# Optimization experiments

Measured on AMD Instinct MI355X. Metric: run time of the kernel, lower is better.

The kernel has to match this reference:

```python
import jax, jax.numpy as jnp
import numpy as np

CAT_SIZES = [31360, 6807, 18, 94]
TOTAL = int(sum(CAT_SIZES))          # 38279
EMB = 128
N_FIELDS = len(CAT_SIZES)
D_IN = N_FIELDS * EMB                # 512 (num_features is empty)
MLP_DIMS = [2048, 1024, 512]
B = 16384
OFFSETS = np.concatenate([[0], np.cumsum(CAT_SIZES)[:-1]]).astype(np.int32)


def setup_inputs() -> dict:
    key = jax.random.key(0)
    ks = jax.random.split(key, 20)
    # x holds raw per-field category ids stored as float32 (as the torch model expects)
    cols = [jax.random.randint(ks[i], (B,), 0, s) for i, s in enumerate(CAT_SIZES)]
    x = jnp.stack(cols, axis=1).astype(jnp.float32)

    bias = jnp.zeros((1,), jnp.float32)
    fc = jax.random.uniform(ks[4], (TOTAL, 1), dtype=jnp.float32)          # nn.Parameter(torch.rand)
    emb_table = jax.random.normal(ks[5], (TOTAL, EMB), dtype=jnp.float32)  # nn.Embedding default N(0,1)

    dims = [D_IN] + MLP_DIMS + [1]
    params = {}
    for i in range(len(dims) - 1):
        fan_in = dims[i]
        bound = 1.0 / np.sqrt(fan_in)
        params[f"W{i+1}"] = jax.random.uniform(ks[6 + 2 * i], (dims[i], dims[i + 1]), jnp.float32, -bound, bound)
        params[f"b{i+1}"] = jax.random.uniform(ks[7 + 2 * i], (dims[i + 1],), jnp.float32, -bound, bound)

    return dict(x=x, bias=bias, fc=fc, emb_table=emb_table, **params)


def reference(x, bias, fc, emb_table, W1, b1, W2, b2, W3, b3, W4, b4):
    cat = x.astype(jnp.int32)                       # [B, F] raw per-field ids
    b = cat.shape[0]

    # embedding lookup with RAW (un-offset) ids, faithful to the original code
    embed_x = emb_table[cat].reshape(b, -1)          # [B, F*EMB]

    # one_hot(offset ids) @ fc  ==  sum_f fc[offset ids]  (offset ranges disjoint)
    gidx = cat + jnp.asarray(OFFSETS)                # [B, F] global ids
    lin = jnp.sum(fc[gidx, 0], axis=1)               # [B]
    fm_y = bias + lin                                # [B]

    # FM term: embed_x is 2-D, so sum over dim=1 collapses features;
    # the keepdim sum over dim=-1 then collapses the BATCH dim to shape (1,)
    # (a quirk of the original code that we reproduce exactly)
    square_of_sum = jnp.sum(embed_x, axis=1) ** 2    # [B]
    sum_of_square = jnp.sum(embed_x ** 2, axis=1)    # [B]
    fm_y = fm_y + 0.5 * jnp.sum(square_of_sum - sum_of_square, axis=-1, keepdims=True)  # [B]
    fm_y = fm_y[:, None]                             # [B,1]

    # MLP (eval mode: dropout is identity)
    h = embed_x
    for W, bb in ((W1, b1), (W2, b2), (W3, b3)):
        h = jax.nn.relu(h @ W + bb)
    mlp_y = h @ W4 + b4                              # [B,1]

    return jax.nn.sigmoid(fm_y + mlp_y)              # [B,1]
```

## Files before the change

kernel.cpp:

```cpp
#include <hip/hip_runtime.h>
#include <hip/hip_fp8.h>
#include <cstdint>


typedef float f32x4 __attribute__((ext_vector_type(4)));
typedef int i32x4 __attribute__((ext_vector_type(4)));
typedef int i32x8 __attribute__((ext_vector_type(8)));

#define GLOAD16(gptr, lptr)                                                \
  __builtin_amdgcn_global_load_lds(                                        \
      (const __attribute__((address_space(1))) void*)(gptr),               \
      (__attribute__((address_space(3))) void*)(lptr), 16, 0, 0)

__device__ inline uint32_t f2fp4(float v) {
  uint32_t s = (__float_as_uint(v) >> 31) << 3;
  float a = fabsf(v);
  uint32_t m;
  if (a < 0.25f) m = 0;
  else if (a < 0.75f) m = 1;
  else if (a < 1.25f) m = 2;
  else if (a < 1.75f) m = 3;
  else if (a < 2.5f)  m = 4;
  else if (a < 3.5f)  m = 5;
  else if (a < 5.0f)  m = 6;
  else m = 7;
  return s | m;
}

__device__ inline uint32_t enc4(float x) {
  float c = fminf(fmaxf(x, 0.5f), 6.0f);
  uint32_t u = __float_as_uint(c);
  u += 0x001FFFFFu + ((u >> 22) & 1u);
  int code = (int)(u >> 22) - 252;
  code = code < 1 ? 1 : code;
  return x < 0.25f ? 0u : (uint32_t)code;
}

static constexpr size_t OFF_LIN  = 0;
static constexpr size_t OFF_PART = 65536;
static constexpr size_t OFF_ACC  = 98304;
static constexpr size_t OFF_EMB  = 262144;
static constexpr size_t OFF_H1   = OFF_EMB + 8388608ull;
static constexpr size_t OFF_H2   = OFF_H1 + 33554432ull;
static constexpr size_t OFF_W1T  = OFF_H2 + 16777216ull;
static constexpr size_t OFF_W2T  = OFF_W1T + 524288ull;
static constexpr size_t OFF_W3T  = OFF_W2T + 1048576ull;

__global__ void prep(const float* __restrict__ W1, const float* __restrict__ W2,
                     const float* __restrict__ W3, uint8_t* __restrict__ W1T,
                     uint8_t* __restrict__ W2T, uint8_t* __restrict__ W3T,
                     const float* __restrict__ x, const float* __restrict__ fc,
                     const float* __restrict__ emb, uint8_t* __restrict__ ebf,
                     float* __restrict__ lin, float* __restrict__ partials,
                     float* __restrict__ dotacc) {
  __shared__ __align__(16) float smem[32 * 33];
  int blk = blockIdx.x;
  int tid = threadIdx.x;
  if (blk < 3584) {
    const float* W;
    uint8_t* WT;
    int K, N, bx, by;
    bool perm;
    if (blk < 1024) {
      W = W1; WT = W1T; K = 512; N = 2048; bx = blk & 63; by = blk >> 6;
      perm = false;
    } else if (blk < 3072) {
      int t = blk - 1024;
      W = W2; WT = W2T; K = 2048; N = 1024; bx = t & 31; by = t >> 5;
      perm = true;
    } else {
      int t = blk - 3072;
      W = W3; WT = W3T; K = 1024; N = 512; bx = t & 15; by = t >> 4;
      perm = true;
    }
    int tx = tid & 31, ty = tid >> 5;
    int n0 = bx * 32, k0 = by * 32;
#pragma unroll
    for (int i = ty; i < 32; i += 8)
      smem[i * 33 + tx] = W[(size_t)(k0 + i) * N + n0 + tx];
    __syncthreads();
    if (tx < 16) {
      int kA = perm ? tx : 2 * tx;
      int kB = perm ? tx + 16 : 2 * tx + 1;
#pragma unroll
      for (int i = ty; i < 32; i += 8) {
        uint32_t lo = f2fp4(smem[kA * 33 + i] * 128.f);
        uint32_t hi = f2fp4(smem[kB * 33 + i] * 128.f);
        WT[(size_t)(n0 + i) * (K >> 1) + (k0 >> 1) + tx] =
            (uint8_t)(lo | (hi << 4));
      }
    }
  } else if (blk < 7680) {
    int gb = blk - 3584;
    int wv = tid >> 6, lane = tid & 63;
    int b = gb * 4 + wv;
    int f = lane >> 4;
    int idx = (int)x[b * 4 + f];
    const float* row = emb + (size_t)idx * 128 + (lane & 15) * 8;
    float4 v0 = ((const float4*)row)[0];
    float4 v1 = ((const float4*)row)[1];
    float s = v0.x + v0.y + v0.z + v0.w + v1.x + v1.y + v1.z + v1.w;
    float q = v0.x * v0.x + v0.y * v0.y + v0.z * v0.z + v0.w * v0.w +
              v1.x * v1.x + v1.y * v1.y + v1.z * v1.z + v1.w * v1.w;

    uint32_t b0 = f2fp4(v0.x * 2.f) | (f2fp4(v0.y * 2.f) << 4);
    uint32_t b1 = f2fp4(v0.z * 2.f) | (f2fp4(v0.w * 2.f) << 4);
    uint32_t b2 = f2fp4(v1.x * 2.f) | (f2fp4(v1.y * 2.f) << 4);
    uint32_t b3 = f2fp4(v1.z * 2.f) | (f2fp4(v1.w * 2.f) << 4);
    uint32_t pk = b0 | (b1 << 8) | (b2 << 16) | (b3 << 24);
    *(uint32_t*)(ebf + (size_t)b * 256 + lane * 4) = pk;

    float lp = 0.f;
    if ((lane & 15) == 0) {
      int off = (f == 1) ? 31360 : (f == 2) ? 38167 : (f == 3) ? 38185 : 0;
      lp = fc[idx + off];
    }
#pragma unroll
    for (int m = 32; m; m >>= 1) {
      s += __shfl_xor(s, m);
      q += __shfl_xor(q, m);
      lp += __shfl_xor(lp, m);
    }
    float* pt = smem;
    if (lane == 0) {
      lin[b] = lp;
      pt[wv] = s * s - q;
    }
    __syncthreads();
    if (tid == 0) partials[gb] = pt[0] + pt[1] + pt[2] + pt[3];
  } else {
    int zb = blk - 7680;
    ((float4*)dotacc)[zb * 256 + tid] = make_float4(0.f, 0.f, 0.f, 0.f);
  }
}

template <bool AFP4>
__global__ __launch_bounds__(256, 2) void gemm_mx_q4(
    const uint8_t* __restrict__ A, const uint8_t* __restrict__ BT,
    const float* __restrict__ bias, uint8_t* __restrict__ C, int K, int N,
    int GX, int sa, float osc) {
  constexpr int ABYTES = AFP4 ? 128 : 256;
  __shared__ __align__(16) uint8_t As[128][ABYTES];
  __shared__ __align__(16) uint8_t Bs[256][128];
  int bid = blockIdx.x;
  int by = (bid & 7) + ((bid >> 3) / GX) * 8;
  int bx = (bid >> 3) & (GX - 1);
  int tid = threadIdx.x;
  int wv = tid >> 6, lane = tid & 63;
  int m0 = by * 128, n0 = bx * 256;
  int mw = (wv >> 1) * 64, nw = (wv & 1) * 128;
  int ml = lane & 15, kg = lane >> 4;
  int Kb2 = K >> 1;

  int arow16 = wv * 4 + (lane >> 4);
  int acol16 = ((lane & 15) ^ arow16) * 16;
  int arow8 = lane >> 3;
  int acol8 = ((lane & 7) ^ arow8) * 16;
  int brow = wv * 8 + (lane >> 3);
  int bcol = ((lane & 7) ^ (brow & 7)) * 16;

  f32x4 acc[4][8];
#pragma unroll
  for (int i = 0; i < 4; ++i)
#pragma unroll
    for (int j = 0; j < 8; ++j) acc[i][j] = (f32x4){0.f, 0.f, 0.f, 0.f};

  for (int kt = 0; kt < K; kt += 256) {
    if constexpr (!AFP4) {
#pragma unroll
      for (int r = 0; r < 8; ++r) {
        const uint8_t* ga = A + (size_t)(m0 + r * 16 + arow16) * K + kt + acol16;
        GLOAD16(ga, &As[r * 16 + wv * 4][0]);
      }
    } else {
#pragma unroll
      for (int r = 0; r < 4; ++r) {
        int g = r * 4 + wv;
        const uint8_t* ga =
            A + (size_t)(m0 + 8 * g + arow8) * Kb2 + (kt >> 1) + acol8;
        GLOAD16(ga, &As[8 * g][0]);
      }
    }
#pragma unroll
    for (int r = 0; r < 8; ++r) {
      const uint8_t* gb =
          BT + (size_t)(n0 + r * 32 + brow) * Kb2 + (kt >> 1) + bcol;
      GLOAD16(gb, &Bs[r * 32 + wv * 8][0]);
    }
    __syncthreads();

    i32x4 z = (i32x4){0, 0, 0, 0};
#pragma unroll
    for (int j = 0; j < 2; ++j) {
      int pb = ((4 * j + kg) ^ (ml & 7)) * 16;
      i32x8 af[4];
#pragma unroll
      for (int mt = 0; mt < 4; ++mt) {
        int ra = mw + mt * 16 + ml;
        if constexpr (!AFP4) {
          int pa0 = ((8 * j + 2 * kg) ^ ml) * 16;
          int pa1 = ((8 * j + 2 * kg + 1) ^ ml) * 16;
          i32x4 a0 = *(const i32x4*)&As[ra][pa0];
          i32x4 a1 = *(const i32x4*)&As[ra][pa1];
          af[mt] = __builtin_shufflevector(a0, a1, 0, 1, 2, 3, 4, 5, 6, 7);
        } else {
          int pa = ((4 * j + kg) ^ (ml & 7)) * 16;
          i32x4 a0 = *(const i32x4*)&As[ra][pa];
          af[mt] = __builtin_shufflevector(a0, z, 0, 1, 2, 3, 4, 5, 6, 7);
        }
      }
#pragma unroll
      for (int nt = 0; nt < 8; ++nt) {
        i32x4 vb = *(const i32x4*)&Bs[nw + nt * 16 + ml][pb];
        i32x8 bf = __builtin_shufflevector(vb, z, 0, 1, 2, 3, 4, 5, 6, 7);
#pragma unroll
        for (int mt = 0; mt < 4; ++mt)
          acc[mt][nt] = __builtin_amdgcn_mfma_scale_f32_16x16x128_f8f6f4(
              af[mt], bf, acc[mt][nt],
               AFP4 ? 4 : 0,  4,
              0, sa, 0, 0x78787878);
      }
    }
    __syncthreads();
  }

  int rbase = kg * 4;
  int NB = N >> 1;
  int cb0 = ((n0 + nw) >> 1) + ml;
  float bvo[8];
#pragma unroll
  for (int nt = 0; nt < 8; ++nt) bvo[nt] = bias[n0 + nw + nt * 16 + ml] * osc;
#pragma unroll
  for (int mt = 0; mt < 4; ++mt) {
    int row = m0 + mw + mt * 16 + rbase;
#pragma unroll
    for (int p = 0; p < 4; ++p) {
#pragma unroll
      for (int r = 0; r < 4; ++r) {
        float xl = fmaxf(fmaf(acc[mt][2 * p][r], osc, bvo[2 * p]), 0.f);
        float xh = fmaxf(fmaf(acc[mt][2 * p + 1][r], osc, bvo[2 * p + 1]), 0.f);
        C[(size_t)(row + r) * NB + cb0 + p * 16] =
            (uint8_t)(enc4(xl) | (enc4(xh) << 4));
      }
    }
  }
}

__global__ __launch_bounds__(256, 2) void gemm_mx_dot(
    const uint8_t* __restrict__ A, const uint8_t* __restrict__ BT,
    const float* __restrict__ bias, const float* __restrict__ W4,
    float* __restrict__ dotacc, int K, int N, int GX, int sa) {
  __shared__ __align__(16) uint8_t As[128][128];
  __shared__ __align__(16) uint8_t Bs[256][128];
  int bid = blockIdx.x;
  int by = (bid & 7) + ((bid >> 3) / GX) * 8;
  int bx = (bid >> 3) & (GX - 1);
  int tid = threadIdx.x;
  int wv = tid >> 6, lane = tid & 63;
  int m0 = by * 128, n0 = bx * 256;
  int mw = (wv >> 1) * 64, nw = (wv & 1) * 128;
  int ml = lane & 15, kg = lane >> 4;
  int Kb2 = K >> 1;

  int arow8 = lane >> 3;
  int acol8 = ((lane & 7) ^ arow8) * 16;
  int brow = wv * 8 + (lane >> 3);
  int bcol = ((lane & 7) ^ (brow & 7)) * 16;

  f32x4 acc[4][8];
#pragma unroll
  for (int i = 0; i < 4; ++i)
#pragma unroll
    for (int j = 0; j < 8; ++j) acc[i][j] = (f32x4){0.f, 0.f, 0.f, 0.f};

  for (int kt = 0; kt < K; kt += 256) {
#pragma unroll
    for (int r = 0; r < 4; ++r) {
      int g = r * 4 + wv;
      const uint8_t* ga =
          A + (size_t)(m0 + 8 * g + arow8) * Kb2 + (kt >> 1) + acol8;
      GLOAD16(ga, &As[8 * g][0]);
    }
#pragma unroll
    for (int r = 0; r < 8; ++r) {
      const uint8_t* gb =
          BT + (size_t)(n0 + r * 32 + brow) * Kb2 + (kt >> 1) + bcol;
      GLOAD16(gb, &Bs[r * 32 + wv * 8][0]);
    }
    __syncthreads();

    i32x4 z = (i32x4){0, 0, 0, 0};
#pragma unroll
    for (int j = 0; j < 2; ++j) {
      int pb = ((4 * j + kg) ^ (ml & 7)) * 16;
      i32x8 af[4];
#pragma unroll
      for (int mt = 0; mt < 4; ++mt) {
        int ra = mw + mt * 16 + ml;
        int pa = ((4 * j + kg) ^ (ml & 7)) * 16;
        i32x4 a0 = *(const i32x4*)&As[ra][pa];
        af[mt] = __builtin_shufflevector(a0, z, 0, 1, 2, 3, 4, 5, 6, 7);
      }
#pragma unroll
      for (int nt = 0; nt < 8; ++nt) {
        i32x4 vb = *(const i32x4*)&Bs[nw + nt * 16 + ml][pb];
        i32x8 bf = __builtin_shufflevector(vb, z, 0, 1, 2, 3, 4, 5, 6, 7);
#pragma unroll
        for (int mt = 0; mt < 4; ++mt)
          acc[mt][nt] = __builtin_amdgcn_mfma_scale_f32_16x16x128_f8f6f4(
              af[mt], bf, acc[mt][nt],
               4,  4,
              0, sa, 0, 0x78787878);
      }
    }
    __syncthreads();
  }

  float bv[8], w4v[8];
#pragma unroll
  for (int nt = 0; nt < 8; ++nt) {
    int col = n0 + nw + nt * 16 + ml;
    bv[nt] = bias[col];
    w4v[nt] = W4[col];
  }
  int rbase = kg * 4;
#pragma unroll
  for (int mt = 0; mt < 4; ++mt) {
#pragma unroll
    for (int r = 0; r < 4; ++r) {
      float p = 0.f;
#pragma unroll
      for (int nt = 0; nt < 8; ++nt) {
        float v = acc[mt][nt][r] + bv[nt];
        v = v > 0.f ? v : 0.f;
        p += v * w4v[nt];
      }
#pragma unroll
      for (int m = 1; m < 16; m <<= 1) p += __shfl_xor(p, m);
      if (ml == 0)
        atomicAdd(&dotacc[m0 + mw + mt * 16 + rbase + r], p);
    }
  }
}

__global__ void final_out(const float* __restrict__ part,
                          const float* __restrict__ dotacc,
                          const float* __restrict__ lin,
                          const float* __restrict__ bias,
                          const float* __restrict__ b4,
                          float* __restrict__ out) {
  __shared__ float ps[4];
  int tid = threadIdx.x;
  float v = 0.f;
  for (int i = tid; i < 4096; i += 256) v += part[i];
#pragma unroll
  for (int m = 32; m; m >>= 1) v += __shfl_xor(v, m);
  if ((tid & 63) == 0) ps[tid >> 6] = v;
  __syncthreads();
  float S = ps[0] + ps[1] + ps[2] + ps[3];
  int i = blockIdx.x * 256 + tid;
  float z = dotacc[i] + b4[0] + bias[0] + lin[i] + 0.5f * S;
  out[i] = 1.f / (1.f + expf(-z));
}

extern "C" void kernel_launch(void* const* d_in, const int* in_sizes, int n_in,
                              void* d_out, int out_size, void* d_ws,
                              size_t ws_size, hipStream_t stream) {
  const float* x    = (const float*)d_in[0];
  const float* bias = (const float*)d_in[1];
  const float* fc   = (const float*)d_in[2];
  const float* emb  = (const float*)d_in[3];
  const float* W1   = (const float*)d_in[4];
  const float* b1   = (const float*)d_in[5];
  const float* W2   = (const float*)d_in[6];
  const float* b2   = (const float*)d_in[7];
  const float* W3   = (const float*)d_in[8];
  const float* b3   = (const float*)d_in[9];
  const float* W4   = (const float*)d_in[10];
  const float* b4   = (const float*)d_in[11];
  float* out = (float*)d_out;

  char* ws = (char*)d_ws;
  float* lin    = (float*)(ws + OFF_LIN);
  float* part   = (float*)(ws + OFF_PART);
  float* dacc   = (float*)(ws + OFF_ACC);
  uint8_t* EMBb = (uint8_t*)(ws + OFF_EMB);
  uint8_t* H1   = (uint8_t*)(ws + OFF_H1);
  uint8_t* H2   = (uint8_t*)(ws + OFF_H2);
  uint8_t* W1T  = (uint8_t*)(ws + OFF_W1T);
  uint8_t* W2T  = (uint8_t*)(ws + OFF_W2T);
  uint8_t* W3T  = (uint8_t*)(ws + OFF_W3T);

  prep<<<7696, 256, 0, stream>>>(W1, W2, W3, W1T, W2T, W3T, x, fc, emb, EMBb,
                                 lin, part, dacc);

  gemm_mx_q4<true><<<1024, 256, 0, stream>>>(EMBb, W1T, b1, H1, 512, 2048, 8,
                                             0x7E7E7E7E, 2.0f);
  gemm_mx_q4<true><<<512, 256, 0, stream>>>(H1, W2T, b2, H2, 2048, 1024, 4,
                                            0x7E7E7E7E, 4.0f);
  gemm_mx_dot<<<256, 256, 0, stream>>>(H2, W3T, b3, W4, dacc, 1024, 512, 2,
                                       0x7D7D7D7D);

  final_out<<<64, 256, 0, stream>>>(part, dacc, lin, bias, b4, out);
}
```

Before: 164.7 us.

## Fuse three MLP GEMMs and final output into one cooperative persistent kernel

Replaces four separate kernel launches (layer 1, layer 2, layer 3 dot, and the sigmoid output) with a single cooperative kernel of 512 blocks that loops over tiles and separates stages with grid-wide syncs. The aim is to remove launch gaps and tail effects between the dependent stages. In exchange it adds grid.sync costs and the constraints of a cooperative launch. Stage 3 and the output stage leave most blocks idle, and 512 blocks must all fit co-resident on the device.

```diff
diff --git a/kernel.cpp b/kernel.cpp
--- a/kernel.cpp
+++ b/kernel.cpp
@@ -1,6 +1,9 @@
 #include <hip/hip_runtime.h>
+#include <hip/hip_cooperative_groups.h>
 #include <hip/hip_fp8.h>
 #include <cstdint>
+
+namespace cg = cooperative_groups;
 
 
 typedef float f32x4 __attribute__((ext_vector_type(4)));
@@ -134,134 +137,23 @@
   }
 }
 
-template <bool AFP4>
-__global__ __launch_bounds__(256, 2) void gemm_mx_q4(
-    const uint8_t* __restrict__ A, const uint8_t* __restrict__ BT,
-    const float* __restrict__ bias, uint8_t* __restrict__ C, int K, int N,
-    int GX, int sa, float osc) {
-  constexpr int ABYTES = AFP4 ? 128 : 256;
-  __shared__ __align__(16) uint8_t As[128][ABYTES];
-  __shared__ __align__(16) uint8_t Bs[256][128];
-  int bid = blockIdx.x;
-  int by = (bid & 7) + ((bid >> 3) / GX) * 8;
-  int bx = (bid >> 3) & (GX - 1);
+template <int MODE>
+__device__ __forceinline__ void gemm_tile(
+    uint8_t* SM, const uint8_t* __restrict__ A, const uint8_t* __restrict__ BT,
+    const float* __restrict__ bias, uint8_t* __restrict__ C,
+    const float* __restrict__ W4, float* __restrict__ dotacc,
+    int K, int N, int GX, int sa, float osc, int vt) {
+  uint8_t(*As)[128] = reinterpret_cast<uint8_t(*)[128]>(SM);
+  uint8_t(*Bs)[128] = reinterpret_cast<uint8_t(*)[128]>(SM + 16384);
   int tid = threadIdx.x;
+  int by = (vt & 7) + ((vt >> 3) / GX) * 8;
+  int bx = (vt >> 3) & (GX - 1);
   int wv = tid >> 6, lane = tid & 63;
   int m0 = by * 128, n0 = bx * 256;
   int mw = (wv >> 1) * 64, nw = (wv & 1) * 128;
   int ml = lane & 15, kg = lane >> 4;
   int Kb2 = K >> 1;
 
-  int arow16 = wv * 4 + (lane >> 4);
-  int acol16 = ((lane & 15) ^ arow16) * 16;
-  int arow8 = lane >> 3;
-  int acol8 = ((lane & 7) ^ arow8) * 16;
-  int brow = wv * 8 + (lane >> 3);
-  int bcol = ((lane & 7) ^ (brow & 7)) * 16;
-
-  f32x4 acc[4][8];
-#pragma unroll
-  for (int i = 0; i < 4; ++i)
-#pragma unroll
-    for (int j = 0; j < 8; ++j) acc[i][j] = (f32x4){0.f, 0.f, 0.f, 0.f};
-
-  for (int kt = 0; kt < K; kt += 256) {
-    if constexpr (!AFP4) {
-#pragma unroll
-      for (int r = 0; r < 8; ++r) {
-        const uint8_t* ga = A + (size_t)(m0 + r * 16 + arow16) * K + kt + acol16;
-        GLOAD16(ga, &As[r * 16 + wv * 4][0]);
-      }
-    } else {
-#pragma unroll
-      for (int r = 0; r < 4; ++r) {
-        int g = r * 4 + wv;
-        const uint8_t* ga =
-            A + (size_t)(m0 + 8 * g + arow8) * Kb2 + (kt >> 1) + acol8;
-        GLOAD16(ga, &As[8 * g][0]);
-      }
-    }
-#pragma unroll
-    for (int r = 0; r < 8; ++r) {
-      const uint8_t* gb =
-          BT + (size_t)(n0 + r * 32 + brow) * Kb2 + (kt >> 1) + bcol;
-      GLOAD16(gb, &Bs[r * 32 + wv * 8][0]);
-    }
-    __syncthreads();
-
-    i32x4 z = (i32x4){0, 0, 0, 0};
-#pragma unroll
-    for (int j = 0; j < 2; ++j) {
-      int pb = ((4 * j + kg) ^ (ml & 7)) * 16;
-      i32x8 af[4];
-#pragma unroll
-      for (int mt = 0; mt < 4; ++mt) {
-        int ra = mw + mt * 16 + ml;
-        if constexpr (!AFP4) {
-          int pa0 = ((8 * j + 2 * kg) ^ ml) * 16;
-          int pa1 = ((8 * j + 2 * kg + 1) ^ ml) * 16;
-          i32x4 a0 = *(const i32x4*)&As[ra][pa0];
-          i32x4 a1 = *(const i32x4*)&As[ra][pa1];
-          af[mt] = __builtin_shufflevector(a0, a1, 0, 1, 2, 3, 4, 5, 6, 7);
-        } else {
-          int pa = ((4 * j + kg) ^ (ml & 7)) * 16;
-          i32x4 a0 = *(const i32x4*)&As[ra][pa];
-          af[mt] = __builtin_shufflevector(a0, z, 0, 1, 2, 3, 4, 5, 6, 7);
-        }
-      }
-#pragma unroll
-      for (int nt = 0; nt < 8; ++nt) {
-        i32x4 vb = *(const i32x4*)&Bs[nw + nt * 16 + ml][pb];
-        i32x8 bf = __builtin_shufflevector(vb, z, 0, 1, 2, 3, 4, 5, 6, 7);
-#pragma unroll
-        for (int mt = 0; mt < 4; ++mt)
-          acc[mt][nt] = __builtin_amdgcn_mfma_scale_f32_16x16x128_f8f6f4(
-              af[mt], bf, acc[mt][nt],
-               AFP4 ? 4 : 0,  4,
-              0, sa, 0, 0x78787878);
-      }
-    }
-    __syncthreads();
-  }
-
-  int rbase = kg * 4;
-  int NB = N >> 1;
-  int cb0 = ((n0 + nw) >> 1) + ml;
-  float bvo[8];
-#pragma unroll
-  for (int nt = 0; nt < 8; ++nt) bvo[nt] = bias[n0 + nw + nt * 16 + ml] * osc;
-#pragma unroll
-  for (int mt = 0; mt < 4; ++mt) {
-    int row = m0 + mw + mt * 16 + rbase;
-#pragma unroll
-    for (int p = 0; p < 4; ++p) {
-#pragma unroll
-      for (int r = 0; r < 4; ++r) {
-        float xl = fmaxf(fmaf(acc[mt][2 * p][r], osc, bvo[2 * p]), 0.f);
-        float xh = fmaxf(fmaf(acc[mt][2 * p + 1][r], osc, bvo[2 * p + 1]), 0.f);
-        C[(size_t)(row + r) * NB + cb0 + p * 16] =
-            (uint8_t)(enc4(xl) | (enc4(xh) << 4));
-      }
-    }
-  }
-}
-
-__global__ __launch_bounds__(256, 2) void gemm_mx_dot(
-    const uint8_t* __restrict__ A, const uint8_t* __restrict__ BT,
-    const float* __restrict__ bias, const float* __restrict__ W4,
-    float* __restrict__ dotacc, int K, int N, int GX, int sa) {
-  __shared__ __align__(16) uint8_t As[128][128];
-  __shared__ __align__(16) uint8_t Bs[256][128];
-  int bid = blockIdx.x;
-  int by = (bid & 7) + ((bid >> 3) / GX) * 8;
-  int bx = (bid >> 3) & (GX - 1);
-  int tid = threadIdx.x;
-  int wv = tid >> 6, lane = tid & 63;
-  int m0 = by * 128, n0 = bx * 256;
-  int mw = (wv >> 1) * 64, nw = (wv & 1) * 128;
-  int ml = lane & 15, kg = lane >> 4;
-  int Kb2 = K >> 1;
-
   int arow8 = lane >> 3;
   int acol8 = ((lane & 7) ^ arow8) * 16;
   int brow = wv * 8 + (lane >> 3);
@@ -316,51 +208,98 @@
     __syncthreads();
   }
 
-  float bv[8], w4v[8];
-#pragma unroll
-  for (int nt = 0; nt < 8; ++nt) {
-    int col = n0 + nw + nt * 16 + ml;
-    bv[nt] = bias[col];
-    w4v[nt] = W4[col];
+  int rbase = kg * 4;
+  if constexpr (MODE == 0) {
+    int NB = N >> 1;
+    int cb0 = ((n0 + nw) >> 1) + ml;
+    float bvo[8];
+#pragma unroll
+    for (int nt = 0; nt < 8; ++nt)
+      bvo[nt] = bias[n0 + nw + nt * 16 + ml] * osc;
+#pragma unroll
+    for (int mt = 0; mt < 4; ++mt) {
+      int row = m0 + mw + mt * 16 + rbase;
+#pragma unroll
+      for (int p = 0; p < 4; ++p) {
+#pragma unroll
+        for (int r = 0; r < 4; ++r) {
+          float xl = fmaxf(fmaf(acc[mt][2 * p][r], osc, bvo[2 * p]), 0.f);
+          float xh =
+              fmaxf(fmaf(acc[mt][2 * p + 1][r], osc, bvo[2 * p + 1]), 0.f);
+          C[(size_t)(row + r) * NB + cb0 + p * 16] =
+              (uint8_t)(enc4(xl) | (enc4(xh) << 4));
+        }
+      }
+    }
+  } else {
+    float bv[8], w4v[8];
+#pragma unroll
+    for (int nt = 0; nt < 8; ++nt) {
+      int col = n0 + nw + nt * 16 + ml;
+      bv[nt] = bias[col];
+      w4v[nt] = W4[col];
+    }
+#pragma unroll
+    for (int mt = 0; mt < 4; ++mt) {
+#pragma unroll
+      for (int r = 0; r < 4; ++r) {
+        float p = 0.f;
+#pragma unroll
+        for (int nt = 0; nt < 8; ++nt) {
+          float v = acc[mt][nt][r] + bv[nt];
+          v = v > 0.f ? v : 0.f;
+          p += v * w4v[nt];
+        }
+#pragma unroll
+        for (int m = 1; m < 16; m <<= 1) p += __shfl_xor(p, m);
+        if (ml == 0)
+          atomicAdd(&dotacc[m0 + mw + mt * 16 + rbase + r], p);
+      }
+    }
   }
-  int rbase = kg * 4;
-#pragma unroll
-  for (int mt = 0; mt < 4; ++mt) {
-#pragma unroll
-    for (int r = 0; r < 4; ++r) {
-      float p = 0.f;
-#pragma unroll
-      for (int nt = 0; nt < 8; ++nt) {
-        float v = acc[mt][nt][r] + bv[nt];
-        v = v > 0.f ? v : 0.f;
-        p += v * w4v[nt];
-      }
-#pragma unroll
-      for (int m = 1; m < 16; m <<= 1) p += __shfl_xor(p, m);
-      if (ml == 0)
-        atomicAdd(&dotacc[m0 + mw + mt * 16 + rbase + r], p);
-    }
+}
+
+__global__ __launch_bounds__(256, 2) void fused_mlp(
+    const uint8_t* __restrict__ EMBb, const uint8_t* __restrict__ W1T,
+    const float* __restrict__ b1, uint8_t* __restrict__ H1,
+    const uint8_t* __restrict__ W2T, const float* __restrict__ b2,
+    uint8_t* __restrict__ H2, const uint8_t* __restrict__ W3T,
+    const float* __restrict__ b3, const float* __restrict__ W4,
+    float* __restrict__ dotacc, const float* __restrict__ part,
+    const float* __restrict__ lin, const float* __restrict__ bias,
+    const float* __restrict__ b4, float* __restrict__ out) {
+  __shared__ __align__(16) uint8_t SM[49152];
+  cg::grid_group grid = cg::this_grid();
+  int bid = blockIdx.x;
+  int tid = threadIdx.x;
+
+  for (int vt = bid; vt < 1024; vt += 512)
+    gemm_tile<0>(SM, EMBb, W1T, b1, H1, nullptr, nullptr, 512, 2048, 8,
+                 0x7E7E7E7E, 2.0f, vt);
+  grid.sync();
+
+  gemm_tile<0>(SM, H1, W2T, b2, H2, nullptr, nullptr, 2048, 1024, 4,
+               0x7E7E7E7E, 4.0f, bid);
+  grid.sync();
+
+  if (bid < 256)
+    gemm_tile<1>(SM, H2, W3T, b3, nullptr, W4, dotacc, 1024, 512, 2,
+                 0x7D7D7D7D, 1.0f, bid);
+  grid.sync();
+
+  if (bid < 64) {
+    float* ps = (float*)SM;
+    float v = 0.f;
+    for (int i = tid; i < 4096; i += 256) v += part[i];
+#pragma unroll
+    for (int m = 32; m; m >>= 1) v += __shfl_xor(v, m);
+    if ((tid & 63) == 0) ps[tid >> 6] = v;
+    __syncthreads();
+    float S = ps[0] + ps[1] + ps[2] + ps[3];
+    int i = bid * 256 + tid;
+    float z = dotacc[i] + b4[0] + bias[0] + lin[i] + 0.5f * S;
+    out[i] = 1.f / (1.f + expf(-z));
   }
-}
-
-__global__ void final_out(const float* __restrict__ part,
-                          const float* __restrict__ dotacc,
-                          const float* __restrict__ lin,
-                          const float* __restrict__ bias,
-                          const float* __restrict__ b4,
-                          float* __restrict__ out) {
-  __shared__ float ps[4];
-  int tid = threadIdx.x;
-  float v = 0.f;
-  for (int i = tid; i < 4096; i += 256) v += part[i];
-#pragma unroll
-  for (int m = 32; m; m >>= 1) v += __shfl_xor(v, m);
-  if ((tid & 63) == 0) ps[tid >> 6] = v;
-  __syncthreads();
-  float S = ps[0] + ps[1] + ps[2] + ps[3];
-  int i = blockIdx.x * 256 + tid;
-  float z = dotacc[i] + b4[0] + bias[0] + lin[i] + 0.5f * S;
-  out[i] = 1.f / (1.f + expf(-z));
 }
 
 extern "C" void kernel_launch(void* const* d_in, const int* in_sizes, int n_in,
@@ -394,12 +333,8 @@
   prep<<<7696, 256, 0, stream>>>(W1, W2, W3, W1T, W2T, W3T, x, fc, emb, EMBb,
                                  lin, part, dacc);
 
-  gemm_mx_q4<true><<<1024, 256, 0, stream>>>(EMBb, W1T, b1, H1, 512, 2048, 8,
-                                             0x7E7E7E7E, 2.0f);
-  gemm_mx_q4<true><<<512, 256, 0, stream>>>(H1, W2T, b2, H2, 2048, 1024, 4,
-                                            0x7E7E7E7E, 4.0f);
-  gemm_mx_dot<<<256, 256, 0, stream>>>(H2, W3T, b3, W4, dacc, 1024, 512, 2,
-                                       0x7D7D7D7D);
-
-  final_out<<<64, 256, 0, stream>>>(part, dacc, lin, bias, b4, out);
-}
+  void* args[] = {&EMBb, &W1T, &b1, &H1, &W2T, &b2, &H2, &W3T, &b3,
+                  &W4,   &dacc, &part, &lin, &bias, &b4, &out};
+  hipLaunchCooperativeKernel((const void*)fused_mlp, dim3(512), dim3(256),
+                             args, 0, stream);
+}
```

New measurement: 377.1 us. 2.29x slower.
